# Optimization experiments

Measured on AMD Instinct MI355X. Metric: run time of the kernel, lower is better.

Reference implementation:

```python
import jax, jax.numpy as jnp
import numpy as np

N_HEADS = 16  # init kwarg n_heads
LN_EPS = 1e-5  # torch LayerNorm default eps


def setup_inputs() -> dict:
    key = jax.random.key(0)
    k1, k2, k3 = jax.random.split(key, 3)
    b, s, d = 4, 2048, 1024
    x0 = jax.random.normal(k1, (b, s, d), dtype=jnp.float32)
    # input_maps['x0']: Linear(d, 3*d, bias=False); stored as (in, out) so x @ W_in
    W_in = jax.random.normal(k2, (d, 3 * d), dtype=jnp.float32) * (d ** -0.5)
    # W_o: Linear(d, d, bias=False)
    W_o = jax.random.normal(k3, (d, d), dtype=jnp.float32) * (d ** -0.5)
    # key-padding mask: True = masked. All-valid (zeros) per spec.
    src_mask = jnp.zeros((b, s), dtype=bool)
    return {"x0": x0, "W_in": W_in, "W_o": W_o, "src_mask": src_mask}


def reference(x0, W_in, W_o, src_mask):
    b, s, d = x0.shape
    dh = d // N_HEADS  # per-head dim after chunking q,k,v
    x = jnp.einsum('bsd,de->bse', x0, W_in)  # (b, s, 3d)
    # rearrange 'b s (n_h 3*dh) -> b s n_h (3*dh)' then chunk into q,k,v
    x = x.reshape(b, s, N_HEADS, 3 * dh)
    q, k, v = jnp.split(x, 3, axis=-1)  # each (b, s, n_h, dh)
    logits = jnp.einsum('bqhd,bkhd->bhqk', q, k) * (dh ** -0.5)  # (b, n_h, s, s)
    causal = jnp.triu(jnp.ones((s, s), dtype=bool), k=1)
    mask = src_mask[:, None, None, :] | causal[None, None, :, :]
    logits = jnp.where(mask, -jnp.inf, logits)
    attn = jax.nn.softmax(logits, axis=-1)
    out = jnp.einsum('bhqk,bkhd->bqhd', attn, v).reshape(b, s, d)
    out = jnp.einsum('bsd,de->bse', out, W_o)
    y = out + x0  # residual with X[input_names[0]]
    # LayerNorm(out_dim, elementwise_affine=False)
    mu = jnp.mean(y, axis=-1, keepdims=True)
    var = jnp.var(y, axis=-1, keepdims=True)
    return (y - mu) * jax.lax.rsqrt(var + LN_EPS)
```

## Files before the change

kernel.cpp:

```cpp
#include <hip/hip_runtime.h>
#include <hip/hip_bf16.h>

typedef unsigned short u16;
typedef unsigned int u32;
typedef __attribute__((ext_vector_type(8))) short short8;
typedef __attribute__((ext_vector_type(4))) float f32x4;
typedef __attribute__((ext_vector_type(4))) int i32x4;

__device__ __forceinline__ float b2f(u16 u) {
    union { u32 i; float f; } x; x.i = ((u32)u) << 16; return x.f;
}
__device__ __forceinline__ u16 f2b(float f) {
    union { float f; u32 u; } x; x.f = f;
    u32 r = x.u + 0x7fffu + ((x.u >> 16) & 1u);
    return (u16)(r >> 16);
}
__device__ __forceinline__ u32 pkbf(float a, float b) {
    union { __hip_bfloat162 h; u32 u; } x;
    x.h = __float22bfloat162_rn(make_float2(a, b));
    return x.u;
}
__device__ __forceinline__ void async_cp16(const u16* g, u16* l) {
    __builtin_amdgcn_global_load_lds(
        (const __attribute__((address_space(1))) void*)g,
        (__attribute__((address_space(3))) void*)l, 16, 0, 0);
}

__global__ void probe_dtype(const u16* __restrict__ x, int* __restrict__ flag) {
    int bigf = 0;
    for (int i = threadIdx.x; i < 512; i += 64) {
        float v = fabsf(b2f(x[i]));
        if (!(v <= 1e6f)) bigf = 1;
    }
    int any = __any(bigf);
    if (threadIdx.x == 0) *flag = any ? 1 : 0;
}

__global__ __launch_bounds__(256) void canon(
    const void* __restrict__ src, u16* __restrict__ dst, int n,
    const int* __restrict__ flag)
{
    int i = (blockIdx.x * 256 + threadIdx.x) * 8;
    if (i >= n) return;
    if (*flag) {
        const float* s = (const float*)src + i;
        f32x4 a = *(const f32x4*)s;
        f32x4 b = *(const f32x4*)(s + 4);
        union { i32x4 v; u32 w[4]; } o;
        o.w[0] = pkbf(a[0], a[1]); o.w[1] = pkbf(a[2], a[3]);
        o.w[2] = pkbf(b[0], b[1]); o.w[3] = pkbf(b[2], b[3]);
        *(i32x4*)(dst + i) = o.v;
    } else {
        *(i32x4*)(dst + i) = *(const i32x4*)((const u16*)src + i);
    }
}

__global__ __launch_bounds__(256) void canon_t(
    const void* __restrict__ src, u16* __restrict__ dst, int Mdim, int Ndim,
    const int* __restrict__ flag)
{
    __shared__ __align__(16) u16 t[64 * 72];
    const int m0 = blockIdx.x * 64, n0 = blockIdx.y * 64;
    const int tid = threadIdx.x;
    const bool f = (*flag != 0);
#pragma unroll
    for (int p = 0; p < 2; ++p) {
        int s = tid + p * 256;
        int r = s >> 3, c0 = (s & 7) << 3;
        union { i32x4 v; u32 w[4]; } o;
        if (f) {
            const float* sp = (const float*)src + (size_t)(m0 + r) * Ndim + n0 + c0;
            f32x4 a = *(const f32x4*)sp, b = *(const f32x4*)(sp + 4);
            o.w[0] = pkbf(a[0], a[1]); o.w[1] = pkbf(a[2], a[3]);
            o.w[2] = pkbf(b[0], b[1]); o.w[3] = pkbf(b[2], b[3]);
        } else {
            o.v = *(const i32x4*)((const u16*)src + (size_t)(m0 + r) * Ndim + n0 + c0);
        }
        *(i32x4*)(t + r * 72 + c0) = o.v;
    }
    __syncthreads();
#pragma unroll
    for (int p = 0; p < 2; ++p) {
        int s = tid + p * 256;
        int oc = s >> 3, mc = (s & 7) << 3;
        union { i32x4 v; u16 h[8]; } o;
#pragma unroll
        for (int j = 0; j < 8; ++j) o.h[j] = t[(mc + j) * 72 + oc];
        *(i32x4*)(dst + (size_t)(n0 + oc) * Mdim + m0 + mc) = o.v;
    }
}

__global__ __launch_bounds__(256) void vtrans(
    const u16* __restrict__ qkv, u16* __restrict__ vT)
{
    __shared__ __align__(16) u16 t[64 * 72];
    const int bh = blockIdx.x, b = bh >> 4, h = bh & 15;
    const int s0 = blockIdx.y * 64;
    const int tid = threadIdx.x;
#pragma unroll
    for (int p = 0; p < 2; ++p) {
        int s = tid + p * 256;
        int r = s >> 3, c0 = (s & 7) << 3;
        *(i32x4*)(t + r * 72 + c0) =
            *(const i32x4*)(qkv + (size_t)(b * 2048 + s0 + r) * 3072 + h * 192 + 128 + c0);
    }
    __syncthreads();
#pragma unroll
    for (int p = 0; p < 2; ++p) {
        int s = tid + p * 256;
        int oc = s >> 3, mc = (s & 7) << 3;
        union { i32x4 v; u16 h[8]; } o;
#pragma unroll
        for (int j = 0; j < 8; ++j) o.h[j] = t[(mc + j) * 72 + oc];
        *(i32x4*)(vT + (size_t)(h * 64 + oc) * 8192 + b * 2048 + s0 + mc) = o.v;
    }
}

__global__ __launch_bounds__(256) void gemm_bf16(
    const u16* __restrict__ A, const u16* __restrict__ Bt, u16* __restrict__ C,
    int M, int N, int K)
{
    __shared__ __align__(16) u16 lA[128 * 64];
    __shared__ __align__(16) u16 lB[128 * 64];
    const int tid  = threadIdx.x;
    const int lane = tid & 63;
    const int wave = tid >> 6;
    const int la = lane & 15;
    const int qd = lane >> 4;
    const int m0 = blockIdx.x * 128, n0 = blockIdx.y * 128;
    const int wm = (wave & 1) * 64, wn = (wave >> 1) * 64;

    const int srow = lane >> 3;
    const int scol = ((lane & 7) ^ (lane >> 3)) << 3;
    const u16* gA = A  + (size_t)(m0 + wave * 32 + srow) * K + scol;
    const u16* gB = Bt + (size_t)(n0 + wave * 32 + srow) * K + scol;
    u16* lsA = lA + wave * 32 * 64;
    u16* lsB = lB + wave * 32 * 64;

    f32x4 acc[4][4];
    const f32x4 fz = {0.f, 0.f, 0.f, 0.f};
#pragma unroll
    for (int i = 0; i < 4; ++i)
#pragma unroll
        for (int j = 0; j < 4; ++j) acc[i][j] = fz;

    for (int k0 = 0; k0 < K; k0 += 64) {
        __syncthreads();
#pragma unroll
        for (int c = 0; c < 4; ++c) {
            async_cp16(gA + k0 + (size_t)(c * 8) * K, lsA + c * 8 * 64);
            async_cp16(gB + k0 + (size_t)(c * 8) * K, lsB + c * 8 * 64);
        }
        __syncthreads();

#pragma unroll
        for (int s = 0; s < 2; ++s) {
            short8 af[4], bf[4];
#pragma unroll
            for (int i = 0; i < 4; ++i) {
                int row = wm + i * 16 + la;
                af[i] = *(const short8*)(lA + row * 64 + (((s * 4 + qd) ^ (la & 7)) << 3));
            }
#pragma unroll
            for (int j = 0; j < 4; ++j) {
                int row = wn + j * 16 + la;
                bf[j] = *(const short8*)(lB + row * 64 + (((s * 4 + qd) ^ (la & 7)) << 3));
            }
#pragma unroll
            for (int i = 0; i < 4; ++i)
#pragma unroll
                for (int j = 0; j < 4; ++j)
                    acc[i][j] = __builtin_amdgcn_mfma_f32_16x16x32_bf16(
                        af[i], bf[j], acc[i][j], 0, 0, 0);
        }
    }

#pragma unroll
    for (int i = 0; i < 4; ++i)
#pragma unroll
        for (int j = 0; j < 4; ++j)
#pragma unroll
            for (int r = 0; r < 4; ++r) {
                int row = m0 + wm + i * 16 + qd * 4 + r;
                int col = n0 + wn + j * 16 + la;
                C[(size_t)row * N + col] = f2b(acc[i][j][r]);
            }
}

#define S_LEN 2048
#define D3 3072
#define NEG_BIG (-30000.0f)

__global__ __launch_bounds__(256, 4) void attn_fwd(
    const u16* __restrict__ qkv, const u16* __restrict__ vT,
    u16* __restrict__ outp)
{
    __shared__ __align__(16) u16 Ks[2 * 64 * 64];
    __shared__ __align__(16) u16 Vts[2 * 64 * 64];
    __shared__ __align__(16) u16 Ps[64 * 64];
    const int tid  = threadIdx.x;
    const int lane = tid & 63;
    const int wave = tid >> 6;
    const int la = lane & 15;
    const int qd = lane >> 4;
    const int lin = blockIdx.y * 16 + blockIdx.x;
    const int xcd = lin & 7, idx = lin >> 3;
    const int bh = xcd * 8 + (idx >> 4);
    const int px = idx & 15;
    const int b = bh >> 4, h = bh & 15;
    const size_t rowb = (size_t)b * S_LEN * D3;
    const int hq = h * 192;
    const u16* vTp = vT + (size_t)(h * 64) * 8192 + (size_t)b * 2048;
    const f32x4 fz = {0.f, 0.f, 0.f, 0.f};

    const int srow = tid >> 3;
    const int scol = ((tid & 7) ^ (srow & 7)) << 3;
    const u16* gK = qkv + rowb + (size_t)srow * D3 + hq + 64 + scol;
    const u16* gV = vTp + (size_t)srow * 8192 + scol;

    const int swz = (la & 7);

    int cur = 0;
#pragma unroll
    for (int seg = 0; seg < 2; ++seg) {
        const int qt = seg == 0 ? px : 31 - px;
        const int q0 = qt * 64;
        const int qg = q0 + wave * 16 + la;

        short8 bq[2];
#pragma unroll
        for (int s = 0; s < 2; ++s) {
            union { short8 v; u16 h[8]; } u;
            u.v = *(const short8*)(qkv + rowb + (size_t)qg * D3 + hq + s * 32 + qd * 8);
#pragma unroll
            for (int j = 0; j < 8; ++j) u.h[j] = f2b(b2f(u.h[j]) * 0.125f);
            bq[s] = u.v;
        }

        f32x4 Oacc[4];
#pragma unroll
        for (int jd = 0; jd < 4; ++jd) Oacc[jd] = fz;
        float m_run = NEG_BIG, l_run = 0.f;

        __syncthreads();
#pragma unroll
        for (int c = 0; c < 2; ++c) {
            async_cp16(gK + (size_t)(c * 32) * D3, Ks + cur * 4096 + c * 2048 + wave * 512);
            async_cp16(gV + (size_t)(c * 32) * 8192, Vts + cur * 4096 + c * 2048 + wave * 512);
        }

        for (int kt = 0; kt <= qt; ++kt) {
            const int k0 = kt * 64;
            __syncthreads();
            if (kt < qt) {
                const int kn = k0 + 64;
#pragma unroll
                for (int c = 0; c < 2; ++c) {
                    async_cp16(gK + (size_t)(kn + c * 32) * D3,
                               Ks + (cur ^ 1) * 4096 + c * 2048 + wave * 512);
                    async_cp16(gV + (size_t)(c * 32) * 8192 + kn,
                               Vts + (cur ^ 1) * 4096 + c * 2048 + wave * 512);
                }
            }
            const u16* KsC  = Ks  + cur * 4096;
            const u16* VtsC = Vts + cur * 4096;

            f32x4 sacc[4];
#pragma unroll
            for (int jm = 0; jm < 4; ++jm) sacc[jm] = fz;
            __builtin_amdgcn_s_setprio(1);
#pragma unroll
            for (int s = 0; s < 2; ++s) {
#pragma unroll
                for (int jm = 0; jm < 4; ++jm) {
                    short8 ak = *(const short8*)(KsC + (jm * 16 + la) * 64 +
                                                 (((s * 4 + qd) ^ swz) << 3));
                    sacc[jm] = __builtin_amdgcn_mfma_f32_16x16x32_bf16(ak, bq[s], sacc[jm], 0, 0, 0);
                }
            }
            __builtin_amdgcn_s_setprio(0);
            if (kt == qt) {
#pragma unroll
                for (int jm = 0; jm < 4; ++jm)
#pragma unroll
                    for (int r = 0; r < 4; ++r)
                        if (k0 + jm * 16 + qd * 4 + r > qg) sacc[jm][r] = NEG_BIG;
            }

            float mx = fmaxf(fmaxf(fmaxf(sacc[0][0], sacc[0][1]), fmaxf(sacc[0][2], sacc[0][3])),
                             fmaxf(fmaxf(sacc[1][0], sacc[1][1]), fmaxf(sacc[1][2], sacc[1][3])));
            mx = fmaxf(mx, fmaxf(fmaxf(fmaxf(sacc[2][0], sacc[2][1]), fmaxf(sacc[2][2], sacc[2][3])),
                                 fmaxf(fmaxf(sacc[3][0], sacc[3][1]), fmaxf(sacc[3][2], sacc[3][3]))));
            mx = fmaxf(mx, __shfl_xor(mx, 16));
            mx = fmaxf(mx, __shfl_xor(mx, 32));

            const int skip = __all(mx <= m_run + 4.0f);
            if (!skip) {
                float mnew = fmaxf(m_run, mx);
                float al   = __expf(m_run - mnew);
                float ar[4];
#pragma unroll
                for (int r = 0; r < 4; ++r) ar[r] = __shfl(al, qd * 4 + r);
#pragma unroll
                for (int jd = 0; jd < 4; ++jd)
#pragma unroll
                    for (int r = 0; r < 4; ++r) Oacc[jd][r] *= ar[r];
                l_run *= al;
                m_run = mnew;
            }
            float ssum = 0.f;
#pragma unroll
            for (int jm = 0; jm < 4; ++jm)
#pragma unroll
                for (int r = 0; r < 4; ++r) {
                    float pv = __expf(sacc[jm][r] - m_run);
                    sacc[jm][r] = pv;
                    ssum += pv;
                }
            ssum += __shfl_xor(ssum, 16);
            ssum += __shfl_xor(ssum, 32);
            l_run += ssum;

#pragma unroll
            for (int jm = 0; jm < 4; ++jm) {
                uint2 w;
                w.x = pkbf(sacc[jm][0], sacc[jm][1]);
                w.y = pkbf(sacc[jm][2], sacc[jm][3]);
                *(uint2*)(Ps + (wave * 16 + la) * 64 +
                          ((((jm * 2 + (qd >> 1)) ^ swz)) << 3) + ((qd & 1) << 2)) = w;
            }

            __builtin_amdgcn_s_setprio(1);
#pragma unroll
            for (int s = 0; s < 2; ++s) {
                short8 ap = *(const short8*)(Ps + (wave * 16 + la) * 64 +
                                             (((s * 4 + qd) ^ swz) << 3));
#pragma unroll
                for (int jd = 0; jd < 4; ++jd) {
                    short8 bv = *(const short8*)(VtsC + (jd * 16 + la) * 64 +
                                                 (((s * 4 + qd) ^ swz) << 3));
                    Oacc[jd] = __builtin_amdgcn_mfma_f32_16x16x32_bf16(ap, bv, Oacc[jd], 0, 0, 0);
                }
            }
            __builtin_amdgcn_s_setprio(0);
            cur ^= 1;
        }

#pragma unroll
        for (int r = 0; r < 4; ++r) {
            float lr = __shfl(l_run, qd * 4 + r);
            float inv = 1.f / lr;
            size_t orow = (size_t)(b * S_LEN + q0 + wave * 16 + qd * 4 + r) * 1024 + h * 64;
#pragma unroll
            for (int jd = 0; jd < 4; ++jd)
                outp[orow + jd * 16 + la] = f2b(Oacc[jd][r] * inv);
        }
    }
}

__global__ __launch_bounds__(256) void ln_residual(
    const u16* __restrict__ proj, const u16* __restrict__ x0,
    void* __restrict__ out, const int* __restrict__ flag)
{
    __shared__ float red[8];
    __shared__ float stats[2];
    const size_t base = (size_t)blockIdx.x * 1024 + threadIdx.x * 4;
    union { uint2 u; u16 s[4]; } pa, xa;
    pa.u = *(const uint2*)(proj + base);
    xa.u = *(const uint2*)(x0 + base);
    float y[4];
    float s1 = 0.f, s2 = 0.f;
#pragma unroll
    for (int j = 0; j < 4; ++j) {
        y[j] = b2f(pa.s[j]) + b2f(xa.s[j]);
        s1 += y[j];
        s2 += y[j] * y[j];
    }
#pragma unroll
    for (int off = 32; off > 0; off >>= 1) {
        s1 += __shfl_down(s1, off);
        s2 += __shfl_down(s2, off);
    }
    const int wave = threadIdx.x >> 6, lane = threadIdx.x & 63;
    if (lane == 0) { red[wave * 2] = s1; red[wave * 2 + 1] = s2; }
    __syncthreads();
    if (threadIdx.x == 0) {
        float S1 = red[0] + red[2] + red[4] + red[6];
        float S2 = red[1] + red[3] + red[5] + red[7];
        float mean = S1 * (1.f / 1024.f);
        float var  = fmaxf(S2 * (1.f / 1024.f) - mean * mean, 0.f);
        stats[0] = mean;
        stats[1] = rsqrtf(var + 1e-5f);
    }
    __syncthreads();
    float mean = stats[0], inv = stats[1];
    if (*flag) {
        f32x4 o;
#pragma unroll
        for (int j = 0; j < 4; ++j) o[j] = (y[j] - mean) * inv;
        *(f32x4*)((float*)out + base) = o;
    } else {
        union { uint2 u; u16 s[4]; } o;
#pragma unroll
        for (int j = 0; j < 4; ++j) o.s[j] = f2b((y[j] - mean) * inv);
        *(uint2*)((u16*)out + base) = o.u;
    }
}

extern "C" void kernel_launch(void* const* d_in, const int* in_sizes, int n_in,
                              void* d_out, int out_size, void* d_ws, size_t ws_size,
                              hipStream_t stream) {
    char* ws = (char*)d_ws;
    int* flag = (int*)ws;
    u16* cx0  = (u16*)(ws + 256);
    u16* wtin = cx0  + (size_t)8192 * 1024;
    u16* wto  = wtin + (size_t)3072 * 1024;
    u16* qkv  = wto  + (size_t)1024 * 1024;
    u16* vT   = qkv  + (size_t)8192 * 3072;
    u16* attn = vT   + (size_t)1024 * 8192;
    u16* proj = qkv;

    dim3 blk(256);
    probe_dtype<<<1, 64, 0, stream>>>((const u16*)d_in[0], flag);
    canon<<<4096, blk, 0, stream>>>(d_in[0], cx0, 8192 * 1024, flag);
    canon_t<<<dim3(16, 48), blk, 0, stream>>>(d_in[1], wtin, 1024, 3072, flag);
    canon_t<<<dim3(16, 16), blk, 0, stream>>>(d_in[2], wto,  1024, 1024, flag);
    gemm_bf16<<<dim3(64, 24), blk, 0, stream>>>(cx0, wtin, qkv, 8192, 3072, 1024);
    vtrans<<<dim3(64, 32), blk, 0, stream>>>(qkv, vT);
    attn_fwd<<<dim3(16, 64), blk, 0, stream>>>(qkv, vT, attn);
    gemm_bf16<<<dim3(64, 8), blk, 0, stream>>>(attn, wto, proj, 8192, 1024, 1024);
    ln_residual<<<dim3(8192), blk, 0, stream>>>(proj, cx0, d_out, flag);
}
```

Before: 283.2 us.

## Add 256x256-tile 8-wave GEMM for QKV projection and use exp2 in softmax

Adds a new GEMM kernel with 256x256 output tiles, 512 threads, double-buffered async global-to-LDS loads interleaved with four MFMA quadrants, XCD-aware block swizzle and setprio scheduling. It replaces the 128-tile GEMM for the QKV projection, aiming at more data reuse per LDS byte and better overlap of loads with MFMAs. Separately, the attention softmax exponent is computed as exp2 of an FMA with a prescaled max, saving a subtract and a multiply inside __expf. The large tile raises register and LDS pressure, and gives only 384 workgroups, which may underfill the GPU.

```diff
diff --git a/kernel.cpp b/kernel.cpp
--- a/kernel.cpp
+++ b/kernel.cpp
@@ -187,9 +187,166 @@
             }
 }
 
+__global__ __launch_bounds__(512, 2) void gemm256(
+    const u16* __restrict__ A, const u16* __restrict__ Bt, u16* __restrict__ C,
+    int M, int N, int K)
+{
+    __shared__ __align__(16) u16 sA[2][256 * 64];
+    __shared__ __align__(16) u16 sB[2][256 * 64];
+    const int tid  = threadIdx.x;
+    const int lane = tid & 63;
+    const int wave = tid >> 6;
+    const int la = lane & 15;
+    const int qd = lane >> 4;
+    const int wm = wave >> 2;
+    const int wn = wave & 3;
+
+    const int Mb  = M >> 8;
+    const int nwg = gridDim.x;
+    const int id  = blockIdx.x;
+    const int swz = (id & 7) * (nwg >> 3) + (id >> 3);
+    const int m0 = (swz % Mb) * 256;
+    const int n0 = (swz / Mb) * 256;
+
+    const int srow = tid >> 3;
+    const int scol = (((tid & 7) ^ (srow & 7)) << 3);
+
+    const int nt = K >> 6;
+
+    auto stageA = [&](int tk, int half) {
+        u16* dst = &sA[tk & 1][half * 128 * 64] + tid * 8;
+        const u16* g = A + (size_t)(m0 + half * 128 + srow) * K + tk * 64 + scol;
+        async_cp16(g, dst);
+        async_cp16(g + (size_t)64 * K, dst + 64 * 64);
+    };
+    auto stageB = [&](int tk, int half) {
+        u16* dst = &sB[tk & 1][half * 128 * 64] + tid * 8;
+        const u16* g = Bt + (size_t)(n0 + half * 128 + srow) * K + tk * 64 + scol;
+        async_cp16(g, dst);
+        async_cp16(g + (size_t)64 * K, dst + 64 * 64);
+    };
+
+    f32x4 acc[8][4];
+    const f32x4 fz = {0.f, 0.f, 0.f, 0.f};
+#pragma unroll
+    for (int i = 0; i < 8; ++i)
+#pragma unroll
+        for (int j = 0; j < 4; ++j) acc[i][j] = fz;
+
+    stageA(0, 0); stageA(0, 1); stageB(0, 0); stageB(0, 1);
+    stageA(1, 0); stageA(1, 1);
+    asm volatile("s_waitcnt vmcnt(4)" ::: "memory");
+    __builtin_amdgcn_s_barrier();
+
+    const int swk = (la & 7);
+
+#pragma unroll 2
+    for (int t = 0; t < nt; ++t) {
+        const u16* pA = &sA[t & 1][0];
+        const u16* pB = &sB[t & 1][0];
+        short8 a0[2][4], a1[2][4], b0[2][2], b1[2][2];
+
+#pragma unroll
+        for (int s = 0; s < 2; ++s) {
+#pragma unroll
+            for (int f = 0; f < 4; ++f)
+                a0[s][f] = *(const short8*)(pA + (wm * 128 + f * 16 + la) * 64 +
+                                            (((s * 4 + qd) ^ swk) << 3));
+#pragma unroll
+            for (int f = 0; f < 2; ++f)
+                b0[s][f] = *(const short8*)(pB + (wn * 64 + f * 16 + la) * 64 +
+                                            (((s * 4 + qd) ^ swk) << 3));
+        }
+        if (t + 1 < nt) stageB(t + 1, 0);
+        __builtin_amdgcn_s_barrier();
+        asm volatile("s_waitcnt lgkmcnt(0)" ::: "memory");
+        __builtin_amdgcn_s_setprio(1);
+#pragma unroll
+        for (int s = 0; s < 2; ++s)
+#pragma unroll
+            for (int f = 0; f < 4; ++f)
+#pragma unroll
+                for (int j = 0; j < 2; ++j)
+                    acc[f][j] = __builtin_amdgcn_mfma_f32_16x16x32_bf16(
+                        a0[s][f], b0[s][j], acc[f][j], 0, 0, 0);
+        __builtin_amdgcn_s_setprio(0);
+        __builtin_amdgcn_s_barrier();
+
+#pragma unroll
+        for (int s = 0; s < 2; ++s)
+#pragma unroll
+            for (int f = 0; f < 4; ++f)
+                a1[s][f] = *(const short8*)(pA + (wm * 128 + (4 + f) * 16 + la) * 64 +
+                                            (((s * 4 + qd) ^ swk) << 3));
+        if (t + 1 < nt) stageB(t + 1, 1);
+        __builtin_amdgcn_s_barrier();
+        asm volatile("s_waitcnt lgkmcnt(0)" ::: "memory");
+        __builtin_amdgcn_s_setprio(1);
+#pragma unroll
+        for (int s = 0; s < 2; ++s)
+#pragma unroll
+            for (int f = 0; f < 4; ++f)
+#pragma unroll
+                for (int j = 0; j < 2; ++j)
+                    acc[4 + f][j] = __builtin_amdgcn_mfma_f32_16x16x32_bf16(
+                        a1[s][f], b0[s][j], acc[4 + f][j], 0, 0, 0);
+        __builtin_amdgcn_s_setprio(0);
+        __builtin_amdgcn_s_barrier();
+
+#pragma unroll
+        for (int s = 0; s < 2; ++s)
+#pragma unroll
+            for (int f = 0; f < 2; ++f)
+                b1[s][f] = *(const short8*)(pB + (wn * 64 + (2 + f) * 16 + la) * 64 +
+                                            (((s * 4 + qd) ^ swk) << 3));
+        if (t + 2 < nt) stageA(t + 2, 0);
+        __builtin_amdgcn_s_barrier();
+        asm volatile("s_waitcnt lgkmcnt(0)" ::: "memory");
+        __builtin_amdgcn_s_setprio(1);
+#pragma unroll
+        for (int s = 0; s < 2; ++s)
+#pragma unroll
+            for (int f = 0; f < 4; ++f)
+#pragma unroll
+                for (int j = 0; j < 2; ++j)
+                    acc[f][2 + j] = __builtin_amdgcn_mfma_f32_16x16x32_bf16(
+                        a0[s][f], b1[s][j], acc[f][2 + j], 0, 0, 0);
+        __builtin_amdgcn_s_setprio(0);
+        __builtin_amdgcn_s_barrier();
+
+        if (t + 2 < nt) stageA(t + 2, 1);
+        __builtin_amdgcn_s_barrier();
+        __builtin_amdgcn_s_setprio(1);
+#pragma unroll
+        for (int s = 0; s < 2; ++s)
+#pragma unroll
+            for (int f = 0; f < 4; ++f)
+#pragma unroll
+                for (int j = 0; j < 2; ++j)
+                    acc[4 + f][2 + j] = __builtin_amdgcn_mfma_f32_16x16x32_bf16(
+                        a1[s][f], b1[s][j], acc[4 + f][2 + j], 0, 0, 0);
+        __builtin_amdgcn_s_setprio(0);
+        if (t + 2 < nt)      asm volatile("s_waitcnt vmcnt(4)" ::: "memory");
+        else if (t + 1 < nt) asm volatile("s_waitcnt vmcnt(0)" ::: "memory");
+        __builtin_amdgcn_s_barrier();
+    }
+
+#pragma unroll
+    for (int fi = 0; fi < 8; ++fi)
+#pragma unroll
+        for (int fj = 0; fj < 4; ++fj)
+#pragma unroll
+            for (int r = 0; r < 4; ++r) {
+                int row = m0 + wm * 128 + fi * 16 + qd * 4 + r;
+                int col = n0 + wn * 64 + fj * 16 + la;
+                C[(size_t)row * N + col] = f2b(acc[fi][fj][r]);
+            }
+}
+
 #define S_LEN 2048
 #define D3 3072
 #define NEG_BIG (-30000.0f)
+#define L2E 1.44269504f
 
 __global__ __launch_bounds__(256, 4) void attn_fwd(
     const u16* __restrict__ qkv, const u16* __restrict__ vT,
@@ -308,12 +465,13 @@
                 l_run *= al;
                 m_run = mnew;
             }
+            const float nm2 = m_run * L2E;
             float ssum = 0.f;
 #pragma unroll
             for (int jm = 0; jm < 4; ++jm)
 #pragma unroll
                 for (int r = 0; r < 4; ++r) {
-                    float pv = __expf(sacc[jm][r] - m_run);
+                    float pv = exp2f(fmaf(sacc[jm][r], L2E, -nm2));
                     sacc[jm][r] = pv;
                     ssum += pv;
                 }
@@ -425,7 +583,7 @@
     canon<<<4096, blk, 0, stream>>>(d_in[0], cx0, 8192 * 1024, flag);
     canon_t<<<dim3(16, 48), blk, 0, stream>>>(d_in[1], wtin, 1024, 3072, flag);
     canon_t<<<dim3(16, 16), blk, 0, stream>>>(d_in[2], wto,  1024, 1024, flag);
-    gemm_bf16<<<dim3(64, 24), blk, 0, stream>>>(cx0, wtin, qkv, 8192, 3072, 1024);
+    gemm256<<<dim3(384), dim3(512), 0, stream>>>(cx0, wtin, qkv, 8192, 3072, 1024);
     vtrans<<<dim3(64, 32), blk, 0, stream>>>(qkv, vT);
     attn_fwd<<<dim3(16, 64), blk, 0, stream>>>(qkv, vT, attn);
     gemm_bf16<<<dim3(64, 8), blk, 0, stream>>>(attn, wto, proj, 8192, 1024, 1024);
```

After: 295.8 us. 4.4% more time.

## Replace GEMM with 256x128-tile multi-buffered async-pipelined kernel

Applied to the files above, without the earlier changes.

Replaces the 128x128 single-buffered GEMM with a 512-thread kernel using 256x128 tiles. A is triple-buffered and B double-buffered in LDS, with async global-to-LDS prefetch kept two steps ahead and explicit vmcnt/lgkmcnt waits. It also adds a block-ID swizzle for L2 locality and raises wave priority during the MFMA bursts. The goal is to hide global load latency behind compute instead of stalling on a barrier every K step. The cost is more LDS per block (about 112KB), which limits occupancy.

```diff
diff --git a/kernel.cpp b/kernel.cpp
--- a/kernel.cpp
+++ b/kernel.cpp
@@ -116,26 +116,48 @@
     }
 }
 
-__global__ __launch_bounds__(256) void gemm_bf16(
+__global__ __launch_bounds__(512, 2) void gemm_bp(
     const u16* __restrict__ A, const u16* __restrict__ Bt, u16* __restrict__ C,
     int M, int N, int K)
 {
-    __shared__ __align__(16) u16 lA[128 * 64];
-    __shared__ __align__(16) u16 lB[128 * 64];
+    __shared__ __align__(16) u16 sA0[256 * 64], sA1[256 * 64], sA2[256 * 64];
+    __shared__ __align__(16) u16 sB0[128 * 64], sB1[128 * 64];
     const int tid  = threadIdx.x;
     const int lane = tid & 63;
     const int wave = tid >> 6;
     const int la = lane & 15;
     const int qd = lane >> 4;
-    const int m0 = blockIdx.x * 128, n0 = blockIdx.y * 128;
-    const int wm = (wave & 1) * 64, wn = (wave >> 1) * 64;
-
-    const int srow = lane >> 3;
-    const int scol = ((lane & 7) ^ (lane >> 3)) << 3;
-    const u16* gA = A  + (size_t)(m0 + wave * 32 + srow) * K + scol;
-    const u16* gB = Bt + (size_t)(n0 + wave * 32 + srow) * K + scol;
-    u16* lsA = lA + wave * 32 * 64;
-    u16* lsB = lB + wave * 32 * 64;
+    const int wm = wave >> 1;
+    const int wn = wave & 1;
+
+    const int Mb  = M >> 8;
+    const int nwg = gridDim.x;
+    const int id  = blockIdx.x;
+    const int swz = (id & 7) * (nwg >> 3) + (id >> 3);
+    const int m0 = (swz % Mb) * 256;
+    const int n0 = (swz / Mb) * 128;
+
+    const int srow = tid >> 3;
+    const int scol = (((tid & 7) ^ (srow & 7)) << 3);
+    const int nt = K >> 6;
+
+    const u16* gA = A  + (size_t)(m0 + srow) * K + scol;
+    const u16* gB = Bt + (size_t)(n0 + srow) * K + scol;
+
+    auto stageA = [&](int tk, u16* buf) {
+        u16* dst = buf + tid * 8;
+        const u16* g = gA + tk * 64;
+#pragma unroll
+        for (int h = 0; h < 4; ++h)
+            async_cp16(g + (size_t)(h * 64) * K, dst + h * 64 * 64);
+    };
+    auto stageB = [&](int tk, u16* buf) {
+        u16* dst = buf + tid * 8;
+        const u16* g = gB + tk * 64;
+#pragma unroll
+        for (int h = 0; h < 2; ++h)
+            async_cp16(g + (size_t)(h * 64) * K, dst + h * 64 * 64);
+    };
 
     f32x4 acc[4][4];
     const f32x4 fz = {0.f, 0.f, 0.f, 0.f};
@@ -144,46 +166,75 @@
 #pragma unroll
         for (int j = 0; j < 4; ++j) acc[i][j] = fz;
 
-    for (int k0 = 0; k0 < K; k0 += 64) {
-        __syncthreads();
-#pragma unroll
-        for (int c = 0; c < 4; ++c) {
-            async_cp16(gA + k0 + (size_t)(c * 8) * K, lsA + c * 8 * 64);
-            async_cp16(gB + k0 + (size_t)(c * 8) * K, lsB + c * 8 * 64);
-        }
-        __syncthreads();
-
-#pragma unroll
-        for (int s = 0; s < 2; ++s) {
-            short8 af[4], bf[4];
-#pragma unroll
-            for (int i = 0; i < 4; ++i) {
-                int row = wm + i * 16 + la;
-                af[i] = *(const short8*)(lA + row * 64 + (((s * 4 + qd) ^ (la & 7)) << 3));
-            }
-#pragma unroll
-            for (int j = 0; j < 4; ++j) {
-                int row = wn + j * 16 + la;
-                bf[j] = *(const short8*)(lB + row * 64 + (((s * 4 + qd) ^ (la & 7)) << 3));
-            }
-#pragma unroll
-            for (int i = 0; i < 4; ++i)
-#pragma unroll
-                for (int j = 0; j < 4; ++j)
-                    acc[i][j] = __builtin_amdgcn_mfma_f32_16x16x32_bf16(
-                        af[i], bf[j], acc[i][j], 0, 0, 0);
-        }
-    }
-
-#pragma unroll
-    for (int i = 0; i < 4; ++i)
-#pragma unroll
-        for (int j = 0; j < 4; ++j)
+    u16 *aCur = sA0, *aNxt = sA1, *aNN = sA2;
+    u16 *bCur = sB0, *bNxt = sB1;
+
+    stageA(0, aCur); stageB(0, bCur); stageA(1, aNxt);
+    asm volatile("s_waitcnt vmcnt(4)" ::: "memory");
+    __builtin_amdgcn_s_barrier();
+
+    const int swk = la & 7;
+
+    for (int t = 0; t < nt; ++t) {
+        short8 a0[4], b0[4];
+#pragma unroll
+        for (int f = 0; f < 4; ++f)
+            a0[f] = *(const short8*)(aCur + (wm * 64 + f * 16 + la) * 64 +
+                                     ((qd ^ swk) << 3));
+#pragma unroll
+        for (int f = 0; f < 4; ++f)
+            b0[f] = *(const short8*)(bCur + (wn * 64 + f * 16 + la) * 64 +
+                                     ((qd ^ swk) << 3));
+        if (t + 1 < nt) stageB(t + 1, bNxt);
+        if (t + 2 < nt) stageA(t + 2, aNN);
+        __builtin_amdgcn_s_barrier();
+        asm volatile("s_waitcnt lgkmcnt(0)" ::: "memory");
+        __builtin_amdgcn_s_setprio(1);
+#pragma unroll
+        for (int i = 0; i < 4; ++i)
+#pragma unroll
+            for (int j = 0; j < 4; ++j)
+                acc[i][j] = __builtin_amdgcn_mfma_f32_16x16x32_bf16(
+                    a0[i], b0[j], acc[i][j], 0, 0, 0);
+        __builtin_amdgcn_s_setprio(0);
+        __builtin_amdgcn_s_barrier();
+
+        short8 a1[4], b1[4];
+#pragma unroll
+        for (int f = 0; f < 4; ++f)
+            a1[f] = *(const short8*)(aCur + (wm * 64 + f * 16 + la) * 64 +
+                                     (((4 + qd) ^ swk) << 3));
+#pragma unroll
+        for (int f = 0; f < 4; ++f)
+            b1[f] = *(const short8*)(bCur + (wn * 64 + f * 16 + la) * 64 +
+                                     (((4 + qd) ^ swk) << 3));
+        __builtin_amdgcn_s_barrier();
+        asm volatile("s_waitcnt lgkmcnt(0)" ::: "memory");
+        __builtin_amdgcn_s_setprio(1);
+#pragma unroll
+        for (int i = 0; i < 4; ++i)
+#pragma unroll
+            for (int j = 0; j < 4; ++j)
+                acc[i][j] = __builtin_amdgcn_mfma_f32_16x16x32_bf16(
+                    a1[i], b1[j], acc[i][j], 0, 0, 0);
+        __builtin_amdgcn_s_setprio(0);
+        if (t + 2 < nt)      asm volatile("s_waitcnt vmcnt(4)" ::: "memory");
+        else if (t + 1 < nt) asm volatile("s_waitcnt vmcnt(0)" ::: "memory");
+        __builtin_amdgcn_s_barrier();
+
+        u16* tmp = aCur; aCur = aNxt; aNxt = aNN; aNN = tmp;
+        tmp = bCur; bCur = bNxt; bNxt = tmp;
+    }
+
+#pragma unroll
+    for (int fi = 0; fi < 4; ++fi)
+#pragma unroll
+        for (int fj = 0; fj < 4; ++fj)
 #pragma unroll
             for (int r = 0; r < 4; ++r) {
-                int row = m0 + wm + i * 16 + qd * 4 + r;
-                int col = n0 + wn + j * 16 + la;
-                C[(size_t)row * N + col] = f2b(acc[i][j][r]);
+                int row = m0 + wm * 64 + fi * 16 + qd * 4 + r;
+                int col = n0 + wn * 64 + fj * 16 + la;
+                C[(size_t)row * N + col] = f2b(acc[fi][fj][r]);
             }
 }
 
@@ -425,9 +476,9 @@
     canon<<<4096, blk, 0, stream>>>(d_in[0], cx0, 8192 * 1024, flag);
     canon_t<<<dim3(16, 48), blk, 0, stream>>>(d_in[1], wtin, 1024, 3072, flag);
     canon_t<<<dim3(16, 16), blk, 0, stream>>>(d_in[2], wto,  1024, 1024, flag);
-    gemm_bf16<<<dim3(64, 24), blk, 0, stream>>>(cx0, wtin, qkv, 8192, 3072, 1024);
+    gemm_bp<<<dim3(768), dim3(512), 0, stream>>>(cx0, wtin, qkv, 8192, 3072, 1024);
     vtrans<<<dim3(64, 32), blk, 0, stream>>>(qkv, vT);
     attn_fwd<<<dim3(16, 64), blk, 0, stream>>>(qkv, vT, attn);
-    gemm_bf16<<<dim3(64, 8), blk, 0, stream>>>(attn, wto, proj, 8192, 1024, 1024);
+    gemm_bp<<<dim3(256), dim3(512), 0, stream>>>(attn, wto, proj, 8192, 1024, 1024);
     ln_residual<<<dim3(8192), blk, 0, stream>>>(proj, cx0, d_out, flag);
 }
```

After: 288.0 us. No clear change (+1.7%).
